# Kernel tuning notes

Hardware: AMD Instinct MI355X
Metric: run time of the kernel (lower is better)

The kernel has to match this reference:

```python
import jax, jax.numpy as jnp
import numpy as np

N = 50000      # nodes
E = 600000     # edges
F_IN = 128     # num_features
H = 128        # conv_dim
C = 10         # num_classes


def setup_inputs() -> dict:
    key = jax.random.key(0)
    ks = jax.random.split(key, 16)
    s = 0.05
    return {
        "x": jax.random.normal(ks[0], (N, F_IN), jnp.float32),
        "edge_index": jax.random.randint(ks[1], (2, E), 0, N, dtype=jnp.int32),
        "W1": jax.random.normal(ks[2], (F_IN, H), jnp.float32) * s,
        "b1": jnp.zeros((H,), jnp.float32),
        "W2": jax.random.normal(ks[3], (H, H), jnp.float32) * s,
        "b2": jnp.zeros((H,), jnp.float32),
        "W3": jax.random.normal(ks[4], (H, H), jnp.float32) * s,
        "b3": jnp.zeros((H,), jnp.float32),
        "fw1": jax.random.normal(ks[5], (3 * H, 128), jnp.float32) * s,
        "fb1": jnp.zeros((128,), jnp.float32),
        "fw2": jax.random.normal(ks[6], (128, 64), jnp.float32) * s,
        "fb2": jnp.zeros((64,), jnp.float32),
        "fw3": jax.random.normal(ks[7], (64, C), jnp.float32) * s,
        "fb3": jnp.zeros((C,), jnp.float32),
    }


def reference(x, edge_index, W1, b1, W2, b2, W3, b3, fw1, fb1, fw2, fb2, fw3, fb3):
    n = x.shape[0]
    # GCN normalization with self-loops (improved=False): A_hat = D^-1/2 (A+I) D^-1/2
    loop = jnp.arange(n, dtype=edge_index.dtype)
    src = jnp.concatenate([edge_index[0], loop])   # [E+N]
    tgt = jnp.concatenate([edge_index[1], loop])   # [E+N]
    deg = jax.ops.segment_sum(jnp.ones_like(src, dtype=x.dtype), tgt, num_segments=n)
    dis = jnp.where(deg > 0, jax.lax.rsqrt(jnp.maximum(deg, 1e-12)), 0.0)
    norm = dis[src] * dis[tgt]                     # [E+N]

    def gcn(h, W, b):
        hw = h @ W                                 # [N,H] linear transform first
        msg = norm[:, None] * hw[src]              # gather + edge scale
        return jax.ops.segment_sum(msg, tgt, num_segments=n) + b  # scatter-add

    x1 = jax.nn.relu(gcn(x, W1, b1))
    x2 = jax.nn.relu(gcn(x1, W2, b2))
    x3 = jax.nn.relu(gcn(x2, W3, b3))
    h = jnp.sum(jnp.concatenate([x1, x2, x3], axis=1), axis=0)  # [3H] sum pool
    h = jax.nn.relu(h @ fw1 + fb1)
    h = jax.nn.relu(h @ fw2 + fb2)
    return h @ fw3 + fb3
```

## Files before the change

kernel.cpp:

```cpp
#include <hip/hip_runtime.h>

#define FDIM 128

typedef __attribute__((ext_vector_type(8))) short bf16x8;
typedef __attribute__((ext_vector_type(4))) float f32x4;
typedef __attribute__((ext_vector_type(2))) float f32x2;


__device__ __forceinline__ unsigned int cvt_bf16(float f) {
    unsigned int u = __float_as_uint(f);
    return (u + 0x7fffu + ((u >> 16) & 1u)) >> 16;
}



__global__ void hist_kernel(const int* __restrict__ tgt, int* __restrict__ count, int ne) {
    int e = blockIdx.x * blockDim.x + threadIdx.x;
    if (e < ne) atomicAdd(&count[tgt[e]], 1);
}

__global__ __launch_bounds__(256) void scan1_kernel(const int* __restrict__ count,
                                                    float* __restrict__ dis,
                                                    int* __restrict__ tpre,
                                                    int* __restrict__ bsum, int n) {
    __shared__ int sm[256];
    int tid = threadIdx.x, blk = blockIdx.x;
    int base = blk * 2048 + tid * 8;
    int s = 0;
    #pragma unroll
    for (int q = 0; q < 8; q++) {
        int i = base + q;
        if (i < n) {
            int c = count[i];
            s += c;
            dis[i] = rsqrtf((float)(c + 1));
        }
    }
    sm[tid] = s;
    __syncthreads();
    for (int off = 1; off < 256; off <<= 1) {
        int v = sm[tid];
        int u = (tid >= off) ? sm[tid - off] : 0;
        __syncthreads();
        sm[tid] = v + u;
        __syncthreads();
    }
    tpre[blk * 256 + tid] = (tid == 0) ? 0 : sm[tid - 1];
    if (tid == 255) bsum[blk] = sm[255];
}

__global__ __launch_bounds__(1024) void scan2_kernel(const int* __restrict__ bsum,
                                                     int* __restrict__ bpre,
                                                     int* __restrict__ rowptr,
                                                     float* __restrict__ pool,
                                                     int n, int nb) {
    __shared__ int sm[1024];
    int tid = threadIdx.x;
    if (tid < 384) pool[tid] = 0.f;
    sm[tid] = (tid < nb) ? bsum[tid] : 0;
    __syncthreads();
    for (int off = 1; off < 1024; off <<= 1) {
        int v = sm[tid];
        int u = (tid >= off) ? sm[tid - off] : 0;
        __syncthreads();
        sm[tid] = v + u;
        __syncthreads();
    }
    if (tid < nb) bpre[tid] = (tid == 0) ? 0 : sm[tid - 1];
    if (tid == nb - 1) rowptr[n] = sm[tid];
}

__global__ __launch_bounds__(256) void scan3_kernel(const int* __restrict__ count,
                                                    const int* __restrict__ tpre,
                                                    const int* __restrict__ bpre,
                                                    int* __restrict__ rowptr,
                                                    int* __restrict__ cursor, int n) {
    int tid = threadIdx.x, blk = blockIdx.x;
    int run = bpre[blk] + tpre[blk * 256 + tid];
    int base = blk * 2048 + tid * 8;
    #pragma unroll
    for (int q = 0; q < 8; q++) {
        int i = base + q;
        if (i < n) {
            rowptr[i] = run;
            cursor[i] = run;
            run += count[i];
        }
    }
}

__global__ void fill_kernel(const int* __restrict__ src, const int* __restrict__ tgt,
                            int* __restrict__ cursor, int* __restrict__ csrs, int ne) {
    int e = blockIdx.x * blockDim.x + threadIdx.x;
    if (e < ne) {
        int t = tgt[e];
        int s = src[e];
        int slot = atomicAdd(&cursor[t], 1);
        csrs[slot] = s;
    }
}


__global__ void prep_kernel(const float* __restrict__ x,
                            const float* __restrict__ W1, const float* __restrict__ W2,
                            const float* __restrict__ W3,
                            unsigned* __restrict__ x16,
                            unsigned* __restrict__ B1, unsigned* __restrict__ B2,
                            unsigned* __restrict__ B3,
                            unsigned short* __restrict__ g8,
                            int* __restrict__ count, int n) {
    int i = blockIdx.x * blockDim.x + threadIdx.x;
    int nx = n * 64;
    if (i < nx) {
        int m = i >> 6, u = i & 63;
        float lo = x[(size_t)m * 128 + u];
        float hi = x[(size_t)m * 128 + u + 64];
        x16[i] = cvt_bf16(lo) | (cvt_bf16(hi) << 16);
        if (i < n) count[i] = 0;
    } else {
        int k = i - nx;
        if (k < 3 * 8192) {
            int w = k >> 13;
            int jj = k & 8191;
            const float* W = (w == 0) ? W1 : (w == 1) ? W2 : W3;
            unsigned* B    = (w == 0) ? B1 : (w == 1) ? B2 : B3;
            int nn = jj >> 6, u = jj & 63;
            float lo = W[(size_t)u * 128 + nn];
            float hi = W[(size_t)(u + 64) * 128 + nn];
            B[jj] = cvt_bf16(lo) | (cvt_bf16(hi) << 16);
        } else if (k < 3 * 8192 + 64) {
            g8[(size_t)n * 64 + (k - 3 * 8192)] = 0;
        }
    }
}


__global__ __launch_bounds__(256) void gemm_kernel(const unsigned* __restrict__ A16,
                                                   const unsigned* __restrict__ Bt16,
                                                   const float* __restrict__ dis,
                                                   unsigned short* __restrict__ g8, int n) {
    int tid  = threadIdx.x;
    int wave = tid >> 6, lane = tid & 63;
    int quad = lane >> 4, r16 = lane & 15;
    int m0 = (blockIdx.x * 4 + wave) * 16;
    if (m0 >= n) return;

    f32x4 acc[8] = {};

    #pragma unroll
    for (int ks = 0; ks < 4; ks++) {
        int m = m0 + r16;
        if (m >= n) m = n - 1;
        uint4 av = *(const uint4*)(A16 + (size_t)m * 64 + ks * 16 + quad * 4);
        bf16x8 af = *(bf16x8*)&av;
        #pragma unroll
        for (int t = 0; t < 8; t++) {
            int ncol = t * 16 + r16;
            uint4 bv = *(const uint4*)(Bt16 + (size_t)ncol * 64 + ks * 16 + quad * 4);
            bf16x8 bf = *(bf16x8*)&bv;
            acc[t] = __builtin_amdgcn_mfma_f32_16x16x32_bf16(af, bf, acc[t], 0, 0, 0);
        }
    }

    #pragma unroll
    for (int r = 0; r < 4; r++) {
        int row = m0 + quad * 4 + r;
        if (row < n) {
            float dr = dis[row];
            #pragma unroll
            for (int t = 0; t < 4; t++) {
                int p = __builtin_amdgcn_cvt_pk_fp8_f32(dr * acc[t][r], dr * acc[t + 4][r], 0, false);
                g8[(size_t)row * 64 + t * 16 + r16] = (unsigned short)(p & 0xffff);
            }
        }
    }
}


#define AGG_ACC(v)                                                     \
    { f32x2 p;                                                         \
      p = __builtin_amdgcn_cvt_pk_f32_fp8((int)v.x, 0); f0[0]+=p.x; f1[0]+=p.y; \
      p = __builtin_amdgcn_cvt_pk_f32_fp8((int)v.x, 1); f0[1]+=p.x; f1[1]+=p.y; \
      p = __builtin_amdgcn_cvt_pk_f32_fp8((int)v.y, 0); f0[2]+=p.x; f1[2]+=p.y; \
      p = __builtin_amdgcn_cvt_pk_f32_fp8((int)v.y, 1); f0[3]+=p.x; f1[3]+=p.y; \
      p = __builtin_amdgcn_cvt_pk_f32_fp8((int)v.z, 0); f0[4]+=p.x; f1[4]+=p.y; \
      p = __builtin_amdgcn_cvt_pk_f32_fp8((int)v.z, 1); f0[5]+=p.x; f1[5]+=p.y; \
      p = __builtin_amdgcn_cvt_pk_f32_fp8((int)v.w, 0); f0[6]+=p.x; f1[6]+=p.y; \
      p = __builtin_amdgcn_cvt_pk_f32_fp8((int)v.w, 1); f0[7]+=p.x; f1[7]+=p.y; }

#define ISSUE1(buf, ereg, EBASE, mlim)                                 \
    { int e = (EBASE) + j;                                             \
      int s = __shfl(ereg, e);                                         \
      if (e >= (mlim)) s = n;                                          \
      buf = *(const uint4*)(g8 + (size_t)(unsigned)s * 64u + c * 8); }

#define ROUND4(ereg, Q0, mlim)                                         \
    { uint4 u0, u1, u2, u3;                                            \
      ISSUE1(u0, ereg, (Q0) + 0, mlim)                                 \
      if ((mlim) > (Q0) + 8)  ISSUE1(u1, ereg, (Q0) + 8,  mlim)        \
      if ((mlim) > (Q0) + 16) ISSUE1(u2, ereg, (Q0) + 16, mlim)        \
      if ((mlim) > (Q0) + 24) ISSUE1(u3, ereg, (Q0) + 24, mlim)        \
      AGG_ACC(u0)                                                      \
      if ((mlim) > (Q0) + 8)  AGG_ACC(u1)                              \
      if ((mlim) > (Q0) + 16) AGG_ACC(u2)                              \
      if ((mlim) > (Q0) + 24) AGG_ACC(u3) }

__global__ __launch_bounds__(512) void agg_kernel(const unsigned short* __restrict__ g8,
                                                  const float* __restrict__ dis,
                                                  const int* __restrict__ rowptr,
                                                  const int* __restrict__ csrs,
                                                  const float* __restrict__ bias,
                                                  unsigned* __restrict__ out16,
                                                  float* __restrict__ pool, int n) {
    __shared__ float lpool[128];
    int tid = threadIdx.x;
    if (tid < 128) lpool[tid] = 0.f;
    __syncthreads();

    int wave = tid >> 6, lane = tid & 63;
    int j = lane >> 3;
    int c = lane & 7;
    int node0 = (blockIdx.x * 8 + wave) * 4;

    float b0[8], b1[8];
    *(float4*)&b0[0] = *(const float4*)(bias + c * 8);
    *(float4*)&b0[4] = *(const float4*)(bias + c * 8 + 4);
    *(float4*)&b1[0] = *(const float4*)(bias + 64 + c * 8);
    *(float4*)&b1[4] = *(const float4*)(bias + 64 + c * 8 + 4);

    int rpv = 0; float dv = 0.f;
    if (lane <= 4) rpv = rowptr[min(node0 + lane, n)];
    if (lane < 4)  dv  = dis[min(node0 + lane, n - 1)];

    int er[4];
    #pragma unroll
    for (int i = 0; i < 4; i++) {
        int beg = __shfl(rpv, i);
        er[i] = csrs[beg + lane];
    }

    uint4 c0, c1, c2, c3, sB;
    {
        int deg = __shfl(rpv, 1) - __shfl(rpv, 0);
        int mlim = min(deg, 64);
        int ereg = er[0];
        ISSUE1(c0, ereg, 0, mlim)
        if (deg > 8)  ISSUE1(c1, ereg, 8,  mlim)
        if (deg > 16) ISSUE1(c2, ereg, 16, mlim)
        if (deg > 24) ISSUE1(c3, ereg, 24, mlim)
        int s = (node0 < n && j == 0) ? node0 : n;
        sB = *(const uint4*)(g8 + (size_t)(unsigned)s * 64u + c * 8);
    }

    float pp0[8] = {}, pp1[8] = {};

    #pragma unroll
    for (int i = 0; i < 4; i++) {
        int node = node0 + i;
        bool ok = node < n;
        int beg = __shfl(rpv, i);
        int end = __shfl(rpv, i + 1);
        int deg = end - beg;
        float di = __shfl(dv, i);

        float f0[8] = {}, f1[8] = {};
        AGG_ACC(c0)
        if (deg > 8)  AGG_ACC(c1)
        if (deg > 16) AGG_ACC(c2)
        if (deg > 24) AGG_ACC(c3)
        if (deg > 32) {
            int mlim = min(deg, 64);
            ROUND4(er[i], 32, mlim)
            for (int b2 = 64; b2 < deg; b2 += 64) {
                int ereg2 = csrs[beg + b2 + lane];
                int ml2 = min(deg - b2, 64);
                ROUND4(ereg2, 0, ml2)
                if (ml2 > 32) ROUND4(ereg2, 32, ml2)
            }
        }

        uint4 n0v, n1v, n2v, n3v, nS;
        if (i < 3) {
            int nd = __shfl(rpv, i + 2) - end;
            int nml = min(nd, 64);
            int ner = er[i + 1];
            ISSUE1(n0v, ner, 0, nml)
            if (nd > 8)  ISSUE1(n1v, ner, 8,  nml)
            if (nd > 16) ISSUE1(n2v, ner, 16, nml)
            if (nd > 24) ISSUE1(n3v, ner, 24, nml)
            int s = (node + 1 < n && j == 0) ? (node + 1) : n;
            nS = *(const uint4*)(g8 + (size_t)(unsigned)s * 64u + c * 8);
        }

        #pragma unroll
        for (int k = 0; k < 8; k++) {
            f0[k] += __shfl_xor(f0[k], 8);  f1[k] += __shfl_xor(f1[k], 8);
            f0[k] += __shfl_xor(f0[k], 16); f1[k] += __shfl_xor(f1[k], 16);
            f0[k] += __shfl_xor(f0[k], 32); f1[k] += __shfl_xor(f1[k], 32);
        }
        if (j == 0) AGG_ACC(sB)

        if (ok) {
            float r0[8], r1[8];
            #pragma unroll
            for (int k = 0; k < 8; k++) {
                r0[k] = fmaxf(di * f0[k] + b0[k], 0.f);
                r1[k] = fmaxf(di * f1[k] + b1[k], 0.f);
                pp0[k] += r0[k];
                pp1[k] += r1[k];
            }
            if (out16 && j == 0) {
                uint4 wa, wb;
                wa.x = cvt_bf16(r0[0]) | (cvt_bf16(r1[0]) << 16);
                wa.y = cvt_bf16(r0[1]) | (cvt_bf16(r1[1]) << 16);
                wa.z = cvt_bf16(r0[2]) | (cvt_bf16(r1[2]) << 16);
                wa.w = cvt_bf16(r0[3]) | (cvt_bf16(r1[3]) << 16);
                wb.x = cvt_bf16(r0[4]) | (cvt_bf16(r1[4]) << 16);
                wb.y = cvt_bf16(r0[5]) | (cvt_bf16(r1[5]) << 16);
                wb.z = cvt_bf16(r0[6]) | (cvt_bf16(r1[6]) << 16);
                wb.w = cvt_bf16(r0[7]) | (cvt_bf16(r1[7]) << 16);
                *(uint4*)(out16 + (size_t)node * 64 + c * 8)     = wa;
                *(uint4*)(out16 + (size_t)node * 64 + c * 8 + 4) = wb;
            }
        }

        c0 = n0v; c1 = n1v; c2 = n2v; c3 = n3v; sB = nS;
    }

    if (j == 0) {
        #pragma unroll
        for (int k = 0; k < 8; k++) {
            atomicAdd(&lpool[c * 8 + k],      pp0[k]);
            atomicAdd(&lpool[64 + c * 8 + k], pp1[k]);
        }
    }
    __syncthreads();
    if (tid < 128) atomicAdd(&pool[tid], lpool[tid]);
}


__global__ __launch_bounds__(128) void mlp_kernel(const float* __restrict__ pool,
                                                  const float* __restrict__ fw1, const float* __restrict__ fb1,
                                                  const float* __restrict__ fw2, const float* __restrict__ fb2,
                                                  const float* __restrict__ fw3, const float* __restrict__ fb3,
                                                  float* __restrict__ out) {
    __shared__ float h0[384];
    __shared__ float h1[128];
    __shared__ float h2[64];
    int tid = threadIdx.x;
    for (int i = tid; i < 384; i += 128) h0[i] = pool[i];
    __syncthreads();
    {
        float s = fb1[tid];
        for (int k = 0; k < 384; k++) s += h0[k] * fw1[k * 128 + tid];
        h1[tid] = fmaxf(s, 0.f);
    }
    __syncthreads();
    if (tid < 64) {
        float s = fb2[tid];
        for (int k = 0; k < 128; k++) s += h1[k] * fw2[k * 64 + tid];
        h2[tid] = fmaxf(s, 0.f);
    }
    __syncthreads();
    if (tid < 10) {
        float s = fb3[tid];
        for (int k = 0; k < 64; k++) s += h2[k] * fw3[k * 10 + tid];
        out[tid] = s;
    }
}


extern "C" void kernel_launch(void* const* d_in, const int* in_sizes, int n_in,
                              void* d_out, int out_size, void* d_ws, size_t ws_size,
                              hipStream_t stream) {
    const float* x   = (const float*)d_in[0];
    const int*   ei  = (const int*)d_in[1];
    const float* W1  = (const float*)d_in[2];
    const float* b1  = (const float*)d_in[3];
    const float* W2  = (const float*)d_in[4];
    const float* b2  = (const float*)d_in[5];
    const float* W3  = (const float*)d_in[6];
    const float* b3  = (const float*)d_in[7];
    const float* fw1 = (const float*)d_in[8];
    const float* fb1 = (const float*)d_in[9];
    const float* fw2 = (const float*)d_in[10];
    const float* fb2 = (const float*)d_in[11];
    const float* fw3 = (const float*)d_in[12];
    const float* fb3 = (const float*)d_in[13];
    float* out = (float*)d_out;

    const int n  = in_sizes[0] / FDIM;
    const int ne = in_sizes[1] / 2;
    const int* src = ei;
    const int* tgt = ei + ne;

    char* ws = (char*)d_ws;
    size_t packBytes = (size_t)n * 64 * sizeof(unsigned);
    unsigned* x16  = (unsigned*)ws;  ws += packBytes;
    unsigned* A2   = (unsigned*)ws;  ws += packBytes;
    unsigned* A3   = (unsigned*)ws;  ws += packBytes;
    unsigned short* g8 = (unsigned short*)ws; ws += (((size_t)(n + 1) * 64 * 2 + 127) / 128) * 128;
    unsigned* B1t  = (unsigned*)ws;  ws += 128 * 64 * 4;
    unsigned* B2t  = (unsigned*)ws;  ws += 128 * 64 * 4;
    unsigned* B3t  = (unsigned*)ws;  ws += 128 * 64 * 4;
    float* dis  = (float*)ws;        ws += (size_t)n * 4;
    int* count  = (int*)ws;          ws += (size_t)n * 4;
    int* rowptr = (int*)ws;          ws += ((size_t)(n + 4) * 4 / 16) * 16;
    int* cursor = (int*)ws;          ws += (size_t)n * 4;
    int* csrs   = (int*)ws;          ws += (size_t)(ne + 64) * 4;
    float* pool = (float*)ws;        ws += 384 * 4;
    int nb = (n + 2047) / 2048;
    int* tpre = (int*)ws;            ws += (size_t)nb * 256 * 4;
    int* bsum = (int*)ws;            ws += ((size_t)(nb + 3) / 4) * 16;
    int* bpre = (int*)ws;            ws += ((size_t)(nb + 3) / 4) * 16;

    int prepTotal = n * 64 + 3 * 8192 + 64;
    prep_kernel<<<(prepTotal + 255) / 256, 256, 0, stream>>>(x, W1, W2, W3, x16, B1t, B2t, B3t, g8, count, n);

    hist_kernel<<<(ne + 255) / 256, 256, 0, stream>>>(tgt, count, ne);
    scan1_kernel<<<nb, 256, 0, stream>>>(count, dis, tpre, bsum, n);
    scan2_kernel<<<1, 1024, 0, stream>>>(bsum, bpre, rowptr, pool, n, nb);
    scan3_kernel<<<nb, 256, 0, stream>>>(count, tpre, bpre, rowptr, cursor, n);
    fill_kernel<<<(ne + 255) / 256, 256, 0, stream>>>(src, tgt, cursor, csrs, ne);

    int gemmGrid = (n + 63) / 64;
    int aggGrid  = (n + 31) / 32;

    gemm_kernel<<<gemmGrid, 256, 0, stream>>>(x16, B1t, dis, g8, n);
    agg_kernel<<<aggGrid, 512, 0, stream>>>(g8, dis, rowptr, csrs, b1, A2, pool + 0, n);

    gemm_kernel<<<gemmGrid, 256, 0, stream>>>(A2, B2t, dis, g8, n);
    agg_kernel<<<aggGrid, 512, 0, stream>>>(g8, dis, rowptr, csrs, b2, A3, pool + 128, n);

    gemm_kernel<<<gemmGrid, 256, 0, stream>>>(A3, B3t, dis, g8, n);
    agg_kernel<<<aggGrid, 512, 0, stream>>>(g8, dis, rowptr, csrs, b3, (unsigned*)nullptr, pool + 256, n);

    mlp_kernel<<<1, 128, 0, stream>>>(pool, fw1, fb1, fw2, fb2, fw3, fb3, out);
}
```

Baseline: 462.8 us.

## Split aggregation feature dimension into two half-row passes across blocks

Each aggregation block now handles only half of the 128-feature row, 64 bytes of fp8 per node instead of 128, and the grid is doubled so two blocks cover each node group. Each lane loads 8 bytes instead of 16 per neighbor, halving per-thread registers and accumulators. The intent is more parallelism and occupancy for the latency-bound gather. In exchange, CSR indices, rowptr and degree setup are read twice, and the gather issues twice as many smaller, less coalesced requests.

```diff
diff --git a/kernel.cpp b/kernel.cpp
--- a/kernel.cpp
+++ b/kernel.cpp
@@ -182,20 +182,16 @@
       p = __builtin_amdgcn_cvt_pk_f32_fp8((int)v.x, 0); f0[0]+=p.x; f1[0]+=p.y; \
       p = __builtin_amdgcn_cvt_pk_f32_fp8((int)v.x, 1); f0[1]+=p.x; f1[1]+=p.y; \
       p = __builtin_amdgcn_cvt_pk_f32_fp8((int)v.y, 0); f0[2]+=p.x; f1[2]+=p.y; \
-      p = __builtin_amdgcn_cvt_pk_f32_fp8((int)v.y, 1); f0[3]+=p.x; f1[3]+=p.y; \
-      p = __builtin_amdgcn_cvt_pk_f32_fp8((int)v.z, 0); f0[4]+=p.x; f1[4]+=p.y; \
-      p = __builtin_amdgcn_cvt_pk_f32_fp8((int)v.z, 1); f0[5]+=p.x; f1[5]+=p.y; \
-      p = __builtin_amdgcn_cvt_pk_f32_fp8((int)v.w, 0); f0[6]+=p.x; f1[6]+=p.y; \
-      p = __builtin_amdgcn_cvt_pk_f32_fp8((int)v.w, 1); f0[7]+=p.x; f1[7]+=p.y; }
+      p = __builtin_amdgcn_cvt_pk_f32_fp8((int)v.y, 1); f0[3]+=p.x; f1[3]+=p.y; }
 
 #define ISSUE1(buf, ereg, EBASE, mlim)                                 \
     { int e = (EBASE) + j;                                             \
       int s = __shfl(ereg, e);                                         \
       if (e >= (mlim)) s = n;                                          \
-      buf = *(const uint4*)(g8 + (size_t)(unsigned)s * 64u + c * 8); }
+      buf = *(const uint2*)(gp + (size_t)(unsigned)s * 64u + c * 4); }
 
 #define ROUND4(ereg, Q0, mlim)                                         \
-    { uint4 u0, u1, u2, u3;                                            \
+    { uint2 u0, u1, u2, u3;                                            \
       ISSUE1(u0, ereg, (Q0) + 0, mlim)                                 \
       if ((mlim) > (Q0) + 8)  ISSUE1(u1, ereg, (Q0) + 8,  mlim)        \
       if ((mlim) > (Q0) + 16) ISSUE1(u2, ereg, (Q0) + 16, mlim)        \
@@ -217,16 +213,18 @@
     if (tid < 128) lpool[tid] = 0.f;
     __syncthreads();
 
+    int pass = blockIdx.x & 1;
+    int blk  = blockIdx.x >> 1;
     int wave = tid >> 6, lane = tid & 63;
     int j = lane >> 3;
     int c = lane & 7;
-    int node0 = (blockIdx.x * 8 + wave) * 4;
-
-    float b0[8], b1[8];
-    *(float4*)&b0[0] = *(const float4*)(bias + c * 8);
-    *(float4*)&b0[4] = *(const float4*)(bias + c * 8 + 4);
-    *(float4*)&b1[0] = *(const float4*)(bias + 64 + c * 8);
-    *(float4*)&b1[4] = *(const float4*)(bias + 64 + c * 8 + 4);
+    int node0 = (blk * 8 + wave) * 4;
+    const unsigned short* gp = g8 + pass * 32;
+
+    int ub = pass * 32 + c * 4;
+    float b0[4], b1[4];
+    *(float4*)&b0[0] = *(const float4*)(bias + ub);
+    *(float4*)&b1[0] = *(const float4*)(bias + 64 + ub);
 
     int rpv = 0; float dv = 0.f;
     if (lane <= 4) rpv = rowptr[min(node0 + lane, n)];
@@ -239,7 +237,7 @@
         er[i] = csrs[beg + lane];
     }
 
-    uint4 c0, c1, c2, c3, sB;
+    uint2 c0, c1, c2, c3, sB;
     {
         int deg = __shfl(rpv, 1) - __shfl(rpv, 0);
         int mlim = min(deg, 64);
@@ -249,10 +247,10 @@
         if (deg > 16) ISSUE1(c2, ereg, 16, mlim)
         if (deg > 24) ISSUE1(c3, ereg, 24, mlim)
         int s = (node0 < n && j == 0) ? node0 : n;
-        sB = *(const uint4*)(g8 + (size_t)(unsigned)s * 64u + c * 8);
-    }
-
-    float pp0[8] = {}, pp1[8] = {};
+        sB = *(const uint2*)(gp + (size_t)(unsigned)s * 64u + c * 4);
+    }
+
+    float pp0[4] = {}, pp1[4] = {};
 
     #pragma unroll
     for (int i = 0; i < 4; i++) {
@@ -263,7 +261,7 @@
         int deg = end - beg;
         float di = __shfl(dv, i);
 
-        float f0[8] = {}, f1[8] = {};
+        float f0[4] = {}, f1[4] = {};
         AGG_ACC(c0)
         if (deg > 8)  AGG_ACC(c1)
         if (deg > 16) AGG_ACC(c2)
@@ -279,7 +277,7 @@
             }
         }
 
-        uint4 n0v, n1v, n2v, n3v, nS;
+        uint2 n0v, n1v, n2v, n3v, nS;
         if (i < 3) {
             int nd = __shfl(rpv, i + 2) - end;
             int nml = min(nd, 64);
@@ -289,11 +287,11 @@
             if (nd > 16) ISSUE1(n2v, ner, 16, nml)
             if (nd > 24) ISSUE1(n3v, ner, 24, nml)
             int s = (node + 1 < n && j == 0) ? (node + 1) : n;
-            nS = *(const uint4*)(g8 + (size_t)(unsigned)s * 64u + c * 8);
+            nS = *(const uint2*)(gp + (size_t)(unsigned)s * 64u + c * 4);
         }
 
         #pragma unroll
-        for (int k = 0; k < 8; k++) {
+        for (int k = 0; k < 4; k++) {
             f0[k] += __shfl_xor(f0[k], 8);  f1[k] += __shfl_xor(f1[k], 8);
             f0[k] += __shfl_xor(f0[k], 16); f1[k] += __shfl_xor(f1[k], 16);
             f0[k] += __shfl_xor(f0[k], 32); f1[k] += __shfl_xor(f1[k], 32);
@@ -301,26 +299,21 @@
         if (j == 0) AGG_ACC(sB)
 
         if (ok) {
-            float r0[8], r1[8];
+            float r0[4], r1[4];
             #pragma unroll
-            for (int k = 0; k < 8; k++) {
+            for (int k = 0; k < 4; k++) {
                 r0[k] = fmaxf(di * f0[k] + b0[k], 0.f);
                 r1[k] = fmaxf(di * f1[k] + b1[k], 0.f);
                 pp0[k] += r0[k];
                 pp1[k] += r1[k];
             }
             if (out16 && j == 0) {
-                uint4 wa, wb;
+                uint4 wa;
                 wa.x = cvt_bf16(r0[0]) | (cvt_bf16(r1[0]) << 16);
                 wa.y = cvt_bf16(r0[1]) | (cvt_bf16(r1[1]) << 16);
                 wa.z = cvt_bf16(r0[2]) | (cvt_bf16(r1[2]) << 16);
                 wa.w = cvt_bf16(r0[3]) | (cvt_bf16(r1[3]) << 16);
-                wb.x = cvt_bf16(r0[4]) | (cvt_bf16(r1[4]) << 16);
-                wb.y = cvt_bf16(r0[5]) | (cvt_bf16(r1[5]) << 16);
-                wb.z = cvt_bf16(r0[6]) | (cvt_bf16(r1[6]) << 16);
-                wb.w = cvt_bf16(r0[7]) | (cvt_bf16(r1[7]) << 16);
-                *(uint4*)(out16 + (size_t)node * 64 + c * 8)     = wa;
-                *(uint4*)(out16 + (size_t)node * 64 + c * 8 + 4) = wb;
+                *(uint4*)(out16 + (size_t)node * 64 + ub) = wa;
             }
         }
 
@@ -329,9 +322,9 @@
 
     if (j == 0) {
         #pragma unroll
-        for (int k = 0; k < 8; k++) {
-            atomicAdd(&lpool[c * 8 + k],      pp0[k]);
-            atomicAdd(&lpool[64 + c * 8 + k], pp1[k]);
+        for (int k = 0; k < 4; k++) {
+            atomicAdd(&lpool[ub + k],      pp0[k]);
+            atomicAdd(&lpool[64 + ub + k], pp1[k]);
         }
     }
     __syncthreads();
@@ -424,7 +417,7 @@
     fill_kernel<<<(ne + 255) / 256, 256, 0, stream>>>(src, tgt, cursor, csrs, ne);
 
     int gemmGrid = (n + 63) / 64;
-    int aggGrid  = (n + 31) / 32;
+    int aggGrid  = 2 * ((n + 31) / 32);
 
     gemm_kernel<<<gemmGrid, 256, 0, stream>>>(x16, B1t, dis, g8, n);
     agg_kernel<<<aggGrid, 512, 0, stream>>>(g8, dis, rowptr, csrs, b1, A2, pool + 0, n);
```

New measurement: 577.0 us. 24.7% more time.
